# Kernel tuning notes

Hardware: AMD Instinct MI355X
Metric: run time of the kernel (lower is better)

The kernel has to match this reference:

```python
import jax, jax.numpy as jnp
import numpy as np

B, S, H = 2, 2048, 2048
NH = 16
HD = H // NH  # 128


def setup_inputs() -> dict:
    key = jax.random.key(0)
    ks = jax.random.split(key, 10)
    std = 0.02
    hidden_states = jax.random.normal(ks[0], (B, S, H), dtype=jnp.float32)
    # causal additive mask, broadcastable to [B, NH, S, S]
    causal = jnp.tril(jnp.ones((S, S), dtype=jnp.float32))
    attention_mask = jnp.where(causal == 1, 0.0, -1e9)[None, None, :, :] * jnp.ones((B, 1, 1, 1), jnp.float32)
    Wq = jax.random.normal(ks[1], (H, H), jnp.float32) * std
    Wk = jax.random.normal(ks[2], (H, H), jnp.float32) * std
    Wv = jax.random.normal(ks[3], (H, H), jnp.float32) * std
    Wo = jax.random.normal(ks[4], (H, H), jnp.float32) * std
    bq = jnp.zeros((H,), jnp.float32)
    bk = jnp.zeros((H,), jnp.float32)
    bv = jnp.zeros((H,), jnp.float32)
    bo = jnp.zeros((H,), jnp.float32)
    return {"hidden_states": hidden_states, "attention_mask": attention_mask,
            "Wq": Wq, "bq": bq, "Wk": Wk, "bk": bk, "Wv": Wv, "bv": bv, "Wo": Wo, "bo": bo}


def reference(hidden_states, attention_mask, Wq, bq, Wk, bk, Wv, bv, Wo, bo):
    b, s, _ = hidden_states.shape
    q = (hidden_states @ Wq + bq).reshape(b, s, NH, HD)
    k = (hidden_states @ Wk + bk).reshape(b, s, NH, HD)
    v = (hidden_states @ Wv + bv).reshape(b, s, NH, HD)
    # [b, h, s_q, s_k]
    scores = jnp.einsum('bqhd,bkhd->bhqk', q, k) / jnp.sqrt(jnp.float32(HD))
    scores = scores + attention_mask
    probs = jax.nn.softmax(scores, axis=-1)
    out = jnp.einsum('bhqk,bkhd->bqhd', probs, v).reshape(b, s, H)
    return out @ Wo + bo
```

## Files before the change

kernel.cpp:

```cpp
#include <hip/hip_runtime.h>
#include <hip/hip_bf16.h>
#include <stdint.h>

#define SEQ 2048
#define HID 2048
#define NHEAD 16
#define HDIM 128

typedef __attribute__((ext_vector_type(8))) short short8;
typedef __attribute__((ext_vector_type(4))) float f32x4;

__device__ __forceinline__ short f2bf(float f) {
  union { float f; unsigned u; } x; x.f = f;
  unsigned r = (x.u + 0x7FFFu + ((x.u >> 16) & 1u)) >> 16;
  return (short)r;
}

__device__ __forceinline__ void async_ld16(const void* g, void* l) {
  __builtin_amdgcn_global_load_lds(
      (__attribute__((address_space(1))) void*)g,
      (__attribute__((address_space(3))) void*)l, 16, 0, 0);
}

__global__ __launch_bounds__(256) void k_convert(const float* __restrict__ X,
                                                 short* __restrict__ Xb) {
  int i = blockIdx.x * 256 + threadIdx.x;
  float4 v = ((const float4*)X)[i];
  short4 o;
  o.x = f2bf(v.x); o.y = f2bf(v.y); o.z = f2bf(v.z); o.w = f2bf(v.w);
  ((short4*)Xb)[i] = o;
}

__global__ __launch_bounds__(256) void k_transpose(const float* __restrict__ W0,
                                                   const float* __restrict__ W1,
                                                   const float* __restrict__ W2,
                                                   const float* __restrict__ W3,
                                                   short* __restrict__ Wt) {
  __shared__ float t[32][33];
  int z = blockIdx.z;
  const float* W = (z == 0) ? W0 : (z == 1) ? W1 : (z == 2) ? W2 : W3;
  short* o = Wt + (size_t)z * HID * HID;
  int k0 = blockIdx.x * 32, n0 = blockIdx.y * 32;
  int tx = threadIdx.x, ty = threadIdx.y;
  for (int i = 0; i < 4; ++i) {
    int r = ty + i * 8;
    t[r][tx] = W[(size_t)(k0 + r) * HID + n0 + tx];
  }
  __syncthreads();
  for (int i = 0; i < 4; ++i) {
    int r = ty + i * 8;
    o[(size_t)(n0 + r) * HID + k0 + tx] = f2bf(t[tx][r]);
  }
}

__global__ __launch_bounds__(256, 3) void k_gemm_qkv(const short* __restrict__ A,
                                                     const short* __restrict__ Bt,
                                                     const float* __restrict__ bqp,
                                                     const float* __restrict__ bkp,
                                                     const float* __restrict__ bvp,
                                                     short* __restrict__ Qb,
                                                     short* __restrict__ Kb,
                                                     short* __restrict__ VtG) {
  __shared__ short smem[128 * 136];
  short* As = smem;
  short* Bs = smem + 128 * 64;
  const int tid = threadIdx.x;
  const int wave = tid >> 6, lane = tid & 63;
  const int col = lane & 15, quad = lane >> 4;
  const int wm = wave >> 1, wn = wave & 1;
  const int m0 = blockIdx.y * 128;
  const int n0g = blockIdx.x * 128;
  const int j = n0g >> 11;
  const int n0 = n0g & 2047;
  const int K = HID;
  const float* bias = (j == 0) ? bqp : (j == 1) ? bkp : bvp;

  const int rS = (lane >> 3), cS = lane & 7;
  f32x4 acc[4][4];
  for (int i = 0; i < 4; ++i)
    for (int jj = 0; jj < 4; ++jj)
      acc[i][jj] = (f32x4){0.f, 0.f, 0.f, 0.f};

  for (int k0 = 0; k0 < K; k0 += 64) {
    __syncthreads();
    for (int i = 0; i < 4; ++i) {
      int rowb = wave * 8 + i * 32;
      int row = rowb + rS;
      int src = cS ^ (row & 7);
      async_ld16(A + (size_t)(m0 + row) * K + k0 + src * 8,
                 (char*)As + (size_t)rowb * 128);
      async_ld16(Bt + (size_t)(n0g + row) * K + k0 + src * 8,
                 (char*)Bs + (size_t)rowb * 128);
    }
    __syncthreads();
    for (int h = 0; h < 2; ++h) {
      short8 af[4], bf[4];
      for (int mi = 0; mi < 4; ++mi)
        af[mi] = *(const short8*)(As + (wm * 64 + mi * 16 + col) * 64 +
                                  ((h * 4 + quad) ^ (col & 7)) * 8);
      for (int ni = 0; ni < 4; ++ni)
        bf[ni] = *(const short8*)(Bs + (wn * 64 + ni * 16 + col) * 64 +
                                  ((h * 4 + quad) ^ (col & 7)) * 8);
      for (int mi = 0; mi < 4; ++mi)
        for (int ni = 0; ni < 4; ++ni)
          acc[mi][ni] =
              __builtin_amdgcn_mfma_f32_16x16x32_bf16(af[mi], bf[ni], acc[mi][ni], 0, 0, 0);
    }
  }

  __syncthreads();
  short* T = smem;
  if (j == 2) {
    for (int ni = 0; ni < 4; ++ni) {
      int n = wn * 64 + ni * 16 + col;
      float bv = bias[n0 + n];
      for (int mi = 0; mi < 4; ++mi)
        for (int r = 0; r < 4; ++r) {
          int m = wm * 64 + mi * 16 + quad * 4 + r;
          T[n * 136 + m] = f2bf(acc[mi][ni][r] + bv);
        }
    }
    __syncthreads();
    int h = n0 >> 7;
    int b = m0 >> 11, s0l = m0 & 2047;
    int rr = tid >> 1, halfc = tid & 1;
    short* o = VtG + ((size_t)(b * NHEAD + h) * HDIM + rr) * SEQ + s0l;
    for (int i = 0; i < 8; ++i) {
      int chunk = halfc * 8 + i;
      short8 v = *(const short8*)(T + rr * 136 + chunk * 8);
      *(short8*)(o + chunk * 8) = v;
    }
    return;
  }

  for (int ni = 0; ni < 4; ++ni) {
    int n = wn * 64 + ni * 16 + col;
    float bv = bias[n0 + n];
    for (int mi = 0; mi < 4; ++mi)
      for (int r = 0; r < 4; ++r) {
        int m = wm * 64 + mi * 16 + quad * 4 + r;
        T[m * 136 + n] = f2bf(acc[mi][ni][r] + bv);
      }
  }
  __syncthreads();
  short* out = (j == 0) ? Qb : Kb;
  int h = n0 >> 7;
  for (int i = 0; i < 8; ++i) {
    int c = i * 256 + tid;
    int m = c >> 4, ch = c & 15;
    int mm = m0 + m;
    int b = mm >> 11, s = mm & 2047;
    short8 v = *(const short8*)(T + m * 136 + ch * 8);
    *(short8*)(out + ((size_t)(b * NHEAD + h) * SEQ + s) * HDIM + ch * 8) = v;
  }
}

__global__ __launch_bounds__(256, 3) void k_gemm_o(const short* __restrict__ A,
                                                   const short* __restrict__ Bt,
                                                   const float* __restrict__ bias,
                                                   float* __restrict__ out) {
  __shared__ short As[128 * 64];
  __shared__ short Bs[128 * 64];
  const int tid = threadIdx.x;
  const int wave = tid >> 6, lane = tid & 63;
  const int col = lane & 15, quad = lane >> 4;
  const int wm = wave >> 1, wn = wave & 1;
  const int m0 = blockIdx.y * 128, n0 = blockIdx.x * 128;
  const int K = HID;
  const int rS = (lane >> 3), cS = lane & 7;

  f32x4 acc[4][4];
  for (int i = 0; i < 4; ++i)
    for (int jj = 0; jj < 4; ++jj)
      acc[i][jj] = (f32x4){0.f, 0.f, 0.f, 0.f};

  for (int k0 = 0; k0 < K; k0 += 64) {
    __syncthreads();
    for (int i = 0; i < 4; ++i) {
      int rowb = wave * 8 + i * 32;
      int row = rowb + rS;
      int src = cS ^ (row & 7);
      async_ld16(A + (size_t)(m0 + row) * K + k0 + src * 8,
                 (char*)As + (size_t)rowb * 128);
      async_ld16(Bt + (size_t)(n0 + row) * K + k0 + src * 8,
                 (char*)Bs + (size_t)rowb * 128);
    }
    __syncthreads();
    for (int h = 0; h < 2; ++h) {
      short8 af[4], bf[4];
      for (int mi = 0; mi < 4; ++mi)
        af[mi] = *(const short8*)(As + (wm * 64 + mi * 16 + col) * 64 +
                                  ((h * 4 + quad) ^ (col & 7)) * 8);
      for (int ni = 0; ni < 4; ++ni)
        bf[ni] = *(const short8*)(Bs + (wn * 64 + ni * 16 + col) * 64 +
                                  ((h * 4 + quad) ^ (col & 7)) * 8);
      for (int mi = 0; mi < 4; ++mi)
        for (int ni = 0; ni < 4; ++ni)
          acc[mi][ni] =
              __builtin_amdgcn_mfma_f32_16x16x32_bf16(af[mi], bf[ni], acc[mi][ni], 0, 0, 0);
    }
  }

  for (int ni = 0; ni < 4; ++ni) {
    int n = n0 + wn * 64 + ni * 16 + col;
    float bv = bias[n];
    for (int mi = 0; mi < 4; ++mi)
      for (int r = 0; r < 4; ++r) {
        int m = m0 + wm * 64 + mi * 16 + quad * 4 + r;
        out[(size_t)m * HID + n] = acc[mi][ni][r] + bv;
      }
  }
}

__global__ __launch_bounds__(1024) void k_attn(const short* __restrict__ Qb,
                                               const short* __restrict__ Kb,
                                               const short* __restrict__ VtG,
                                               short* __restrict__ AO) {
  __shared__ short Ks[2][64 * 128];
  __shared__ short Vt[2][128 * 64];
  __shared__ short Pb[16 * 16 * 72];

  const int bx = blockIdx.x;
  const int p = bx & 7;
  const int h = (bx >> 3) & 15;
  const int b = bx >> 7;
  const int tid = threadIdx.x;
  const int wave = tid >> 6, lane = tid & 63;
  const int col = lane & 15, quad = lane >> 4;

  const bool hiw = wave < 8;
  const int wslot = wave & 7;
  const int qb = hiw ? (15 - p) : p;
  const int q0 = qb * 128 + wslot * 16;
  const int nt_w = 2 * qb + 2;
  const int nt = 2 * (15 - p) + 2;

  const size_t ho = (size_t)(b * NHEAD + h) * SEQ * HDIM;
  const short* Qh = Qb + ho;
  const short* Kh = Kb + ho;
  const short* Vh = VtG + ho;

  const float scale = 0.08838834764831845f;
  short8 ones;
  for (int i = 0; i < 8; ++i) ones[i] = (short)0x3F80;

  const int rowK = tid >> 4, c16 = tid & 15;
  const int srcK = c16 ^ (rowK & 7);
  const int rowV = tid >> 3, c8 = tid & 7;
  const int srcV = c8 ^ (rowV & 7);
  short* Pw = Pb + wave * 16 * 72;

  short8 qf[4];
  for (int f = 0; f < 4; ++f)
    qf[f] = *(const short8*)(Qh + (size_t)(q0 + col) * HDIM + f * 32 + quad * 8);

  f32x4 o[8], osum;
  for (int t = 0; t < 8; ++t) o[t] = (f32x4){0.f, 0.f, 0.f, 0.f};
  osum = (f32x4){0.f, 0.f, 0.f, 0.f};

  async_ld16(Kh + (size_t)rowK * HDIM + srcK * 8, (char*)Ks[0] + tid * 16);
  async_ld16(Vh + (size_t)rowV * SEQ + srcV * 8, (char*)Vt[0] + tid * 16);

  for (int kb = 0; kb < nt; ++kb) {
    __syncthreads();
    const int cur = kb & 1;
    if (kb + 1 < nt) {
      async_ld16(Kh + (size_t)((kb + 1) * 64 + rowK) * HDIM + srcK * 8,
                 (char*)Ks[cur ^ 1] + tid * 16);
      async_ld16(Vh + (size_t)rowV * SEQ + (kb + 1) * 64 + srcV * 8,
                 (char*)Vt[cur ^ 1] + tid * 16);
    }
    if (kb >= nt_w) continue;

    const short* KsC = Ks[cur];
    const short* VtC = Vt[cur];

    f32x4 s[4];
    for (int nf = 0; nf < 4; ++nf) s[nf] = (f32x4){0.f, 0.f, 0.f, 0.f};
    for (int f = 0; f < 4; ++f)
      for (int nf = 0; nf < 4; ++nf) {
        short8 kf = *(const short8*)(KsC + (nf * 16 + col) * 128 +
                                     (((f * 4 + quad) ^ (col & 7)) * 8));
        s[nf] = __builtin_amdgcn_mfma_f32_16x16x32_bf16(qf[f], kf, s[nf], 0, 0, 0);
      }

    const bool diag = (kb >= 2 * qb);
    for (int nf = 0; nf < 4; ++nf)
      for (int r = 0; r < 4; ++r) {
        float e = __expf(s[nf][r] * scale - 8.0f);
        if (diag) {
          int key = kb * 64 + nf * 16 + col;
          int q = q0 + quad * 4 + r;
          if (key > q) e = 0.f;
        }
        Pw[(quad * 4 + r) * 72 + nf * 16 + col] = f2bf(e);
      }

    for (int kk = 0; kk < 2; ++kk) {
      short8 pa = *(const short8*)(Pw + col * 72 + kk * 32 + quad * 8);
      osum = __builtin_amdgcn_mfma_f32_16x16x32_bf16(pa, ones, osum, 0, 0, 0);
      for (int t = 0; t < 8; ++t) {
        short8 vf = *(const short8*)(VtC + (t * 16 + col) * 64 +
                                     (((kk * 4 + quad) ^ (col & 7)) * 8));
        o[t] = __builtin_amdgcn_mfma_f32_16x16x32_bf16(pa, vf, o[t], 0, 0, 0);
      }
    }
  }

  for (int r = 0; r < 4; ++r) {
    float inv = 1.f / osum[r];
    int q = q0 + quad * 4 + r;
    for (int t = 0; t < 8; ++t)
      AO[((size_t)(b * SEQ + q)) * HID + h * HDIM + 16 * t + col] = f2bf(o[t][r] * inv);
  }
}

extern "C" void kernel_launch(void* const* d_in, const int* in_sizes, int n_in,
                              void* d_out, int out_size, void* d_ws, size_t ws_size,
                              hipStream_t stream) {
  const float* X  = (const float*)d_in[0];
  const float* Wq = (const float*)d_in[2];
  const float* bq = (const float*)d_in[3];
  const float* Wk = (const float*)d_in[4];
  const float* bk = (const float*)d_in[5];
  const float* Wv = (const float*)d_in[6];
  const float* bv = (const float*)d_in[7];
  const float* Wo = (const float*)d_in[8];
  const float* bo = (const float*)d_in[9];

  char* ws = (char*)d_ws;
  short* Xb  = (short*)(ws);
  short* Wt  = (short*)(ws + (16ull << 20));
  short* Qb  = (short*)(ws + (48ull << 20));
  short* Kb  = (short*)(ws + (64ull << 20));
  short* VtG = (short*)(ws + (80ull << 20));
  short* AO  = (short*)(ws + (96ull << 20));

  short* Wto = Wt + (size_t)3 * HID * HID;

  k_convert<<<8192, 256, 0, stream>>>(X, Xb);
  k_transpose<<<dim3(64, 64, 4), dim3(32, 8), 0, stream>>>(Wq, Wk, Wv, Wo, Wt);

  k_gemm_qkv<<<dim3(48, 32), 256, 0, stream>>>(Xb, Wt, bq, bk, bv, Qb, Kb, VtG);

  k_attn<<<2 * NHEAD * 8, 1024, 0, stream>>>(Qb, Kb, VtG, AO);

  k_gemm_o<<<dim3(16, 32), 256, 0, stream>>>(AO, Wto, bo, (float*)d_out);
}
```

Before: 377.6 us.

## Give each attention wave 32 query rows to reuse K/V fragments

The attention kernel drops from 16 waves to 8 per block, and each wave now handles two 16-row query tiles instead of one. Each K and V fragment read from LDS feeds two MFMAs, halving LDS fragment traffic per unit of compute, and each thread issues two async loads per tile. The cost is roughly double the accumulator registers per wave and half as many waves per block, which may reduce latency hiding.

Result: slower. 393.3 us (+4.2%).

```diff
diff --git a/kernel.cpp b/kernel.cpp
--- a/kernel.cpp
+++ b/kernel.cpp
@@ -212,13 +212,13 @@
   }
 }
 
-__global__ __launch_bounds__(1024) void k_attn(const short* __restrict__ Qb,
-                                               const short* __restrict__ Kb,
-                                               const short* __restrict__ VtG,
-                                               short* __restrict__ AO) {
+__global__ __launch_bounds__(512) void k_attn(const short* __restrict__ Qb,
+                                              const short* __restrict__ Kb,
+                                              const short* __restrict__ VtG,
+                                              short* __restrict__ AO) {
   __shared__ short Ks[2][64 * 128];
   __shared__ short Vt[2][128 * 64];
-  __shared__ short Pb[16 * 16 * 72];
+  __shared__ short Pb[8 * 32 * 72];
 
   const int bx = blockIdx.x;
   const int p = bx & 7;
@@ -228,10 +228,10 @@
   const int wave = tid >> 6, lane = tid & 63;
   const int col = lane & 15, quad = lane >> 4;
 
-  const bool hiw = wave < 8;
-  const int wslot = wave & 7;
-  const int qb = hiw ? (15 - p) : p;
-  const int q0 = qb * 128 + wslot * 16;
+  const int group = wave >> 2;
+  const int wslot = wave & 3;
+  const int qb = group ? p : (15 - p);
+  const int q0 = qb * 128 + wslot * 32;
   const int nt_w = 2 * qb + 2;
   const int nt = 2 * (15 - p) + 2;
 
@@ -244,75 +244,93 @@
   short8 ones;
   for (int i = 0; i < 8; ++i) ones[i] = (short)0x3F80;
 
-  const int rowK = tid >> 4, c16 = tid & 15;
-  const int srcK = c16 ^ (rowK & 7);
-  const int rowV = tid >> 3, c8 = tid & 7;
-  const int srcV = c8 ^ (rowV & 7);
-  short* Pw = Pb + wave * 16 * 72;
-
-  short8 qf[4];
-  for (int f = 0; f < 4; ++f)
-    qf[f] = *(const short8*)(Qh + (size_t)(q0 + col) * HDIM + f * 32 + quad * 8);
-
-  f32x4 o[8], osum;
-  for (int t = 0; t < 8; ++t) o[t] = (f32x4){0.f, 0.f, 0.f, 0.f};
-  osum = (f32x4){0.f, 0.f, 0.f, 0.f};
-
-  async_ld16(Kh + (size_t)rowK * HDIM + srcK * 8, (char*)Ks[0] + tid * 16);
-  async_ld16(Vh + (size_t)rowV * SEQ + srcV * 8, (char*)Vt[0] + tid * 16);
+  int rowKi[2], srcKi[2], rowVi[2], srcVi[2];
+  for (int i = 0; i < 2; ++i) {
+    int c = i * 512 + tid;
+    rowKi[i] = c >> 4; srcKi[i] = (c & 15) ^ (rowKi[i] & 7);
+    rowVi[i] = c >> 3; srcVi[i] = (c & 7) ^ (rowVi[i] & 7);
+  }
+  short* Pw = Pb + wave * 32 * 72;
+
+  short8 qf[2][4];
+  for (int m = 0; m < 2; ++m)
+    for (int f = 0; f < 4; ++f)
+      qf[m][f] = *(const short8*)(Qh + (size_t)(q0 + m * 16 + col) * HDIM + f * 32 + quad * 8);
+
+  f32x4 o[2][8], osum[2];
+  for (int m = 0; m < 2; ++m) {
+    for (int t = 0; t < 8; ++t) o[m][t] = (f32x4){0.f, 0.f, 0.f, 0.f};
+    osum[m] = (f32x4){0.f, 0.f, 0.f, 0.f};
+  }
+
+  for (int i = 0; i < 2; ++i) {
+    async_ld16(Kh + (size_t)rowKi[i] * HDIM + srcKi[i] * 8,
+               (char*)Ks[0] + (i * 512 + tid) * 16);
+    async_ld16(Vh + (size_t)rowVi[i] * SEQ + srcVi[i] * 8,
+               (char*)Vt[0] + (i * 512 + tid) * 16);
+  }
 
   for (int kb = 0; kb < nt; ++kb) {
     __syncthreads();
     const int cur = kb & 1;
     if (kb + 1 < nt) {
-      async_ld16(Kh + (size_t)((kb + 1) * 64 + rowK) * HDIM + srcK * 8,
-                 (char*)Ks[cur ^ 1] + tid * 16);
-      async_ld16(Vh + (size_t)rowV * SEQ + (kb + 1) * 64 + srcV * 8,
-                 (char*)Vt[cur ^ 1] + tid * 16);
+      for (int i = 0; i < 2; ++i) {
+        async_ld16(Kh + (size_t)((kb + 1) * 64 + rowKi[i]) * HDIM + srcKi[i] * 8,
+                   (char*)Ks[cur ^ 1] + (i * 512 + tid) * 16);
+        async_ld16(Vh + (size_t)rowVi[i] * SEQ + (kb + 1) * 64 + srcVi[i] * 8,
+                   (char*)Vt[cur ^ 1] + (i * 512 + tid) * 16);
+      }
     }
     if (kb >= nt_w) continue;
 
     const short* KsC = Ks[cur];
     const short* VtC = Vt[cur];
 
-    f32x4 s[4];
-    for (int nf = 0; nf < 4; ++nf) s[nf] = (f32x4){0.f, 0.f, 0.f, 0.f};
+    f32x4 s[2][4];
+    for (int m = 0; m < 2; ++m)
+      for (int nf = 0; nf < 4; ++nf) s[m][nf] = (f32x4){0.f, 0.f, 0.f, 0.f};
     for (int f = 0; f < 4; ++f)
       for (int nf = 0; nf < 4; ++nf) {
         short8 kf = *(const short8*)(KsC + (nf * 16 + col) * 128 +
                                      (((f * 4 + quad) ^ (col & 7)) * 8));
-        s[nf] = __builtin_amdgcn_mfma_f32_16x16x32_bf16(qf[f], kf, s[nf], 0, 0, 0);
+        s[0][nf] = __builtin_amdgcn_mfma_f32_16x16x32_bf16(qf[0][f], kf, s[0][nf], 0, 0, 0);
+        s[1][nf] = __builtin_amdgcn_mfma_f32_16x16x32_bf16(qf[1][f], kf, s[1][nf], 0, 0, 0);
       }
 
     const bool diag = (kb >= 2 * qb);
-    for (int nf = 0; nf < 4; ++nf)
-      for (int r = 0; r < 4; ++r) {
-        float e = __expf(s[nf][r] * scale - 8.0f);
-        if (diag) {
-          int key = kb * 64 + nf * 16 + col;
-          int q = q0 + quad * 4 + r;
-          if (key > q) e = 0.f;
+    for (int m = 0; m < 2; ++m)
+      for (int nf = 0; nf < 4; ++nf)
+        for (int r = 0; r < 4; ++r) {
+          float e = __expf(s[m][nf][r] * scale - 8.0f);
+          if (diag) {
+            int key = kb * 64 + nf * 16 + col;
+            int q = q0 + m * 16 + quad * 4 + r;
+            if (key > q) e = 0.f;
+          }
+          Pw[(m * 16 + quad * 4 + r) * 72 + nf * 16 + col] = f2bf(e);
         }
-        Pw[(quad * 4 + r) * 72 + nf * 16 + col] = f2bf(e);
-      }
 
     for (int kk = 0; kk < 2; ++kk) {
-      short8 pa = *(const short8*)(Pw + col * 72 + kk * 32 + quad * 8);
-      osum = __builtin_amdgcn_mfma_f32_16x16x32_bf16(pa, ones, osum, 0, 0, 0);
+      short8 pa0 = *(const short8*)(Pw + (0 * 16 + col) * 72 + kk * 32 + quad * 8);
+      short8 pa1 = *(const short8*)(Pw + (1 * 16 + col) * 72 + kk * 32 + quad * 8);
+      osum[0] = __builtin_amdgcn_mfma_f32_16x16x32_bf16(pa0, ones, osum[0], 0, 0, 0);
+      osum[1] = __builtin_amdgcn_mfma_f32_16x16x32_bf16(pa1, ones, osum[1], 0, 0, 0);
       for (int t = 0; t < 8; ++t) {
         short8 vf = *(const short8*)(VtC + (t * 16 + col) * 64 +
                                      (((kk * 4 + quad) ^ (col & 7)) * 8));
-        o[t] = __builtin_amdgcn_mfma_f32_16x16x32_bf16(pa, vf, o[t], 0, 0, 0);
-      }
-    }
-  }
-
-  for (int r = 0; r < 4; ++r) {
-    float inv = 1.f / osum[r];
-    int q = q0 + quad * 4 + r;
-    for (int t = 0; t < 8; ++t)
-      AO[((size_t)(b * SEQ + q)) * HID + h * HDIM + 16 * t + col] = f2bf(o[t][r] * inv);
-  }
+        o[0][t] = __builtin_amdgcn_mfma_f32_16x16x32_bf16(pa0, vf, o[0][t], 0, 0, 0);
+        o[1][t] = __builtin_amdgcn_mfma_f32_16x16x32_bf16(pa1, vf, o[1][t], 0, 0, 0);
+      }
+    }
+  }
+
+  for (int m = 0; m < 2; ++m)
+    for (int r = 0; r < 4; ++r) {
+      float inv = 1.f / osum[m][r];
+      int q = q0 + m * 16 + quad * 4 + r;
+      for (int t = 0; t < 8; ++t)
+        AO[((size_t)(b * SEQ + q)) * HID + h * HDIM + 16 * t + col] = f2bf(o[m][t][r] * inv);
+    }
 }
 
 extern "C" void kernel_launch(void* const* d_in, const int* in_sizes, int n_in,
@@ -343,7 +361,7 @@
 
   k_gemm_qkv<<<dim3(48, 32), 256, 0, stream>>>(Xb, Wt, bq, bk, bv, Qb, Kb, VtG);
 
-  k_attn<<<2 * NHEAD * 8, 1024, 0, stream>>>(Qb, Kb, VtG, AO);
+  k_attn<<<2 * NHEAD * 8, 512, 0, stream>>>(Qb, Kb, VtG, AO);
 
   k_gemm_o<<<dim3(16, 32), 256, 0, stream>>>(AO, Wto, bo, (float*)d_out);
 }
```
